# Optimization experiments

Hardware: AMD Instinct MI355X
Metric: run time of the kernel (lower is better)

Reference implementation:

```python
import jax, jax.numpy as jnp
import numpy as np

INPUT_CHANNELS = 6
RESERVOIR_SIZE = 128
SPECTRAL_RADIUS = 0.9
SPARSITY = 0.8
BATCH = 512
SEQ_LEN = 1024


def setup_inputs() -> dict:
    key = jax.random.key(0)
    kx, kin, kres, kmask = jax.random.split(key, 4)
    x = jax.random.normal(kx, (BATCH, SEQ_LEN, INPUT_CHANNELS), dtype=jnp.float32)
    W_in = jax.random.normal(kin, (INPUT_CHANNELS, RESERVOIR_SIZE), dtype=jnp.float32) * 0.1
    # Sparse reservoir matrix rescaled to the target spectral radius (matches __init__).
    W_res = jax.random.normal(kres, (RESERVOIR_SIZE, RESERVOIR_SIZE), dtype=jnp.float32)
    mask = (jax.random.uniform(kmask, (RESERVOIR_SIZE, RESERVOIR_SIZE)) > SPARSITY).astype(jnp.float32)
    W_res = W_res * mask
    eig = np.abs(np.linalg.eigvals(np.asarray(W_res)))
    radius = float(eig.max())
    if radius > 0:
        W_res = W_res * (SPECTRAL_RADIUS / radius)
    return {"x": x, "W_in": W_in, "W_res": W_res}


def reference(x, W_in, W_res):
    # x: [B, S, C]; h_t = tanh(x_t @ W_in + h_{t-1} @ W_res); returns [B, S, R]
    batch = x.shape[0]
    h0 = jnp.zeros((batch, W_res.shape[0]), dtype=x.dtype)

    def step(h, x_t):
        h_new = jnp.tanh(x_t @ W_in + h @ W_res)
        return h_new, h_new

    _, states = jax.lax.scan(step, h0, jnp.swapaxes(x, 0, 1))  # states: [S, B, R]
    return jnp.swapaxes(states, 0, 1)  # [B, S, R]
```

## Files before the change

kernel.cpp:

```cpp
#include <hip/hip_runtime.h>


#define SEQ 1024
#define CIN 6
#define RES 128

__device__ __forceinline__ float fast_tanh(float x) {
    float e = __builtin_exp2f(x * 2.88539008177793f);
    return 1.0f - 2.0f * __builtin_amdgcn_rcpf(e + 1.0f);
}

__global__ __launch_bounds__(256, 2) void esn_fwd(
    const float* __restrict__ x,
    const float* __restrict__ W_in,
    const float* __restrict__ W_res,
    float* __restrict__ out)
{
    __shared__ float x_lds[SEQ * CIN];
    __shared__ float h_lds[2][RES];

    const int t    = threadIdx.x;
    const int row  = blockIdx.x;
    const int lane = t & 63;
    const int w    = t >> 6;
    const int r    = (w << 5) | (lane & 31);
    const int ks   = lane >> 5;

    const float* xrow = x + (size_t)row * SEQ * CIN;
    for (int i = t; i < SEQ * CIN; i += 256) x_lds[i] = xrow[i];

    float win[CIN];
#pragma unroll
    for (int c = 0; c < CIN; ++c) win[c] = W_in[c * RES + r];

    float wreg[64];
#pragma unroll
    for (int j = 0; j < 64; ++j) wreg[j] = W_res[(64 * ks + j) * RES + r];

    if (lane < 32) h_lds[0][r] = 0.0f;
    __syncthreads();

    float* outp = out + (size_t)row * SEQ * RES + r;

    for (int s = 0; s < SEQ; ++s) {
        const int cur = s & 1;

        float acc;
        {
            const float2* xp = (const float2*)&x_lds[s * CIN];
            float2 a = xp[0], b = xp[1], c2 = xp[2];
            float bias = a.x * win[0] + a.y * win[1] + b.x * win[2]
                       + b.y * win[3] + c2.x * win[4] + c2.y * win[5];
            acc = ks ? 0.0f : bias;
        }

        const float4* hp = (const float4*)&h_lds[cur][ks << 6];
#pragma unroll
        for (int j4 = 0; j4 < 16; ++j4) {
            float4 h4 = hp[j4];
            acc += h4.x * wreg[4 * j4 + 0];
            acc += h4.y * wreg[4 * j4 + 1];
            acc += h4.z * wreg[4 * j4 + 2];
            acc += h4.w * wreg[4 * j4 + 3];
        }

        acc += __shfl_xor(acc, 32, 64);

        if (lane < 32) {
            float y = fast_tanh(acc);
            h_lds[cur ^ 1][r] = y;
            outp[s * RES]     = y;
        }
        __syncthreads();
    }
}

extern "C" void kernel_launch(void* const* d_in, const int* in_sizes, int n_in,
                              void* d_out, int out_size, void* d_ws, size_t ws_size,
                              hipStream_t stream) {
    const float* x     = (const float*)d_in[0];
    const float* W_in  = (const float*)d_in[1];
    const float* W_res = (const float*)d_in[2];
    float* out = (float*)d_out;
    (void)in_sizes; (void)n_in; (void)out_size; (void)d_ws; (void)ws_size;

    esn_fwd<<<512, 256, 0, stream>>>(x, W_in, W_res, out);
}
```

Baseline: 696.3 us.

## Split reservoir matvec four ways per output pair using packed FP32 FMA

```diff
diff --git a/kernel.cpp b/kernel.cpp
--- a/kernel.cpp
+++ b/kernel.cpp
@@ -10,66 +10,85 @@
     return 1.0f - 2.0f * __builtin_amdgcn_rcpf(e + 1.0f);
 }
 
-__global__ __launch_bounds__(256, 2) void esn_fwd(
+__device__ __forceinline__ void pk_fma_blo(float2& acc, float2 h, float2 w) {
+    asm("v_pk_fma_f32 %0, %1, %2, %0 op_sel:[0,0,0] op_sel_hi:[0,1,1]"
+        : "+v"(acc) : "v"(h), "v"(w));
+}
+__device__ __forceinline__ void pk_fma_bhi(float2& acc, float2 h, float2 w) {
+    asm("v_pk_fma_f32 %0, %1, %2, %0 op_sel:[1,0,0] op_sel_hi:[1,1,1]"
+        : "+v"(acc) : "v"(h), "v"(w));
+}
+
+__global__ void esn_fwd(
     const float* __restrict__ x,
     const float* __restrict__ W_in,
     const float* __restrict__ W_res,
     float* __restrict__ out)
 {
     __shared__ float x_lds[SEQ * CIN];
-    __shared__ float h_lds[2][RES];
+    __shared__ __align__(16) float2 h_lds[2][RES / 2];
 
     const int t    = threadIdx.x;
     const int row  = blockIdx.x;
     const int lane = t & 63;
     const int w    = t >> 6;
-    const int r    = (w << 5) | (lane & 31);
-    const int ks   = lane >> 5;
+    const int kq   = (lane >> 4) & 3;
+    const int rp   = (w << 4) | (lane & 15);
+    const int r0   = rp << 1;
 
     const float* xrow = x + (size_t)row * SEQ * CIN;
     for (int i = t; i < SEQ * CIN; i += 256) x_lds[i] = xrow[i];
 
-    float win[CIN];
+    float2 win0 = make_float2(0.f, 0.f), win1 = make_float2(0.f, 0.f);
+    if (kq < 3) {
+        win0 = *(const float2*)&W_in[(2 * kq + 0) * RES + r0];
+        win1 = *(const float2*)&W_in[(2 * kq + 1) * RES + r0];
+    }
+    const int cb = (kq < 3) ? 2 * kq : 0;
+
+    float2 w2[32];
 #pragma unroll
-    for (int c = 0; c < CIN; ++c) win[c] = W_in[c * RES + r];
+    for (int j = 0; j < 32; ++j)
+        w2[j] = *(const float2*)&W_res[(kq * 32 + j) * RES + r0];
 
-    float wreg[64];
-#pragma unroll
-    for (int j = 0; j < 64; ++j) wreg[j] = W_res[(64 * ks + j) * RES + r];
-
-    if (lane < 32) h_lds[0][r] = 0.0f;
+    if (t < 64) h_lds[0][t] = make_float2(0.f, 0.f);
     __syncthreads();
 
-    float* outp = out + (size_t)row * SEQ * RES + r;
+    float* outp = out + (size_t)row * SEQ * RES + r0;
 
     for (int s = 0; s < SEQ; ++s) {
-        const int cur = s & 1;
+        const float4* hp = (const float4*)&h_lds[s & 1][0] + (kq << 3);
 
-        float acc;
-        {
-            const float2* xp = (const float2*)&x_lds[s * CIN];
-            float2 a = xp[0], b = xp[1], c2 = xp[2];
-            float bias = a.x * win[0] + a.y * win[1] + b.x * win[2]
-                       + b.y * win[3] + c2.x * win[4] + c2.y * win[5];
-            acc = ks ? 0.0f : bias;
+        float2 a0 = make_float2(0.f, 0.f), a1 = a0, a2 = a0, a3 = a0;
+
+        float2 xc = *(const float2*)&x_lds[s * CIN + cb];
+        pk_fma_blo(a0, xc, win0);
+        pk_fma_bhi(a1, xc, win1);
+
+#pragma unroll
+        for (int j = 0; j < 8; ++j) {
+            float4 h4 = hp[j];
+            float2 hab = make_float2(h4.x, h4.y);
+            float2 hcd = make_float2(h4.z, h4.w);
+            pk_fma_blo(a0, hab, w2[4 * j + 0]);
+            pk_fma_bhi(a1, hab, w2[4 * j + 1]);
+            pk_fma_blo(a2, hcd, w2[4 * j + 2]);
+            pk_fma_bhi(a3, hcd, w2[4 * j + 3]);
         }
 
-        const float4* hp = (const float4*)&h_lds[cur][ks << 6];
-#pragma unroll
-        for (int j4 = 0; j4 < 16; ++j4) {
-            float4 h4 = hp[j4];
-            acc += h4.x * wreg[4 * j4 + 0];
-            acc += h4.y * wreg[4 * j4 + 1];
-            acc += h4.z * wreg[4 * j4 + 2];
-            acc += h4.w * wreg[4 * j4 + 3];
-        }
+        float accx = (a0.x + a1.x) + (a2.x + a3.x);
+        float accy = (a0.y + a1.y) + (a2.y + a3.y);
 
-        acc += __shfl_xor(acc, 32, 64);
+        accx += __shfl_xor(accx, 16, 64);
+        accy += __shfl_xor(accy, 16, 64);
+        accx += __shfl_xor(accx, 32, 64);
+        accy += __shfl_xor(accy, 32, 64);
 
-        if (lane < 32) {
-            float y = fast_tanh(acc);
-            h_lds[cur ^ 1][r] = y;
-            outp[s * RES]     = y;
+        float2 hv = make_float2(fast_tanh(accx), fast_tanh(accy));
+
+        if (kq == 0) {
+            h_lds[(s & 1) ^ 1][rp] = hv;
+            *(float2*)(outp + (size_t)s * RES) = hv;
         }
         __syncthreads();
     }
```

Measured after the change: 882.9 us. 1.27x slower.
